# Performance work log

Hardware: AMD Instinct MI355X
Metric: run time of the kernel (lower is better)

## Reference

```python
import jax, jax.numpy as jnp
import numpy as np

SIZE = 640
FPN_STRIDES = (8, 16, 32, 64, 128)
REG_MAX = 16
NUM_CLASSES = 80
TOPK = 45


def _build_anchors():
    pts, boxes, strides = [], [], []
    for s in FPN_STRIDES:
        h, w = SIZE // s, SIZE // s
        y, x = np.meshgrid(np.arange(h), np.arange(w), indexing='ij')
        yf = y.ravel().astype(np.float32)
        xf = x.ravel().astype(np.float32)
        pts.append(np.stack([(yf + 0.5) * s, (xf + 0.5) * s], -1))
        boxes.append(np.stack([yf * s, xf * s, (yf + 1) * s, (xf + 1) * s], -1))
        strides.append(np.full(h * w, s, np.float32))
    return (jnp.asarray(np.concatenate(pts), jnp.float32),
            jnp.asarray(np.concatenate(boxes), jnp.float32),
            jnp.asarray(np.concatenate(strides), jnp.float32))


ANCHOR_PTS, ANCHOR_BOXES, STRIDES = _build_anchors()
NUM_ANCHORS = ANCHOR_PTS.shape[0]  # 8525


def _iou(b1, b2):
    # elementwise IoU over trailing dim 4 in (y1, x1, y2, x2); axes are symmetric
    ty = jnp.maximum(b1[..., 0], b2[..., 0])
    tx = jnp.maximum(b1[..., 1], b2[..., 1])
    by = jnp.minimum(b1[..., 2], b2[..., 2])
    bx = jnp.minimum(b1[..., 3], b2[..., 3])
    inter = jnp.clip(by - ty, 0.0) * jnp.clip(bx - tx, 0.0)
    a1 = (b1[..., 2] - b1[..., 0]) * (b1[..., 3] - b1[..., 1])
    a2 = (b2[..., 2] - b2[..., 0]) * (b2[..., 3] - b2[..., 1])
    return inter / (a1 + a2 - inter)


def _assign_single(gt_cls, gt_bbox, pred_d):
    # gt_cls: (N,), gt_bbox: (N,4), pred_d: (4,A)
    A, N, C = NUM_ANCHORS, gt_bbox.shape[0], NUM_CLASSES
    pts, boxes, strides = ANCHOR_PTS, ANCHOR_BOXES, STRIDES
    centers = (gt_bbox[:, :2] + gt_bbox[:, 2:]) / 2
    dist = jnp.linalg.norm(centers[:, None, :] - pts[None, :, :], axis=-1)  # (N,A)
    _, k_ind = jax.lax.top_k(-dist, TOPK)  # (N,K) nearest anchors
    kb = boxes[k_ind]  # (N,K,4)
    Dg = _iou(gt_bbox[:, None, :], kb)  # (N,K)
    tg = Dg.mean(1) + Dg.std(1, ddof=1)  # torch .std() is unbiased
    ap = pts[k_ind]  # (N,K,2)
    inside = ((gt_bbox[:, None, 0] <= ap[..., 0]) & (ap[..., 0] <= gt_bbox[:, None, 2]) &
              (gt_bbox[:, None, 1] <= ap[..., 1]) & (ap[..., 1] <= gt_bbox[:, None, 3]))
    valid = (Dg >= tg[:, None]) & inside  # (N,K)
    n_idx = jnp.broadcast_to(jnp.arange(N, dtype=jnp.int32)[:, None], (N, TOPK))
    pri = jnp.where(valid, n_idx, -1).ravel()
    a_flat = k_ind.ravel()
    win_d = jnp.full((A,), -1, jnp.int32).at[a_flat].max(pri)
    wb = gt_bbox[jnp.clip(win_d, 0)]  # (A,4)
    gt_d = jnp.stack([(pts[:, 0] - wb[:, 0]) / strides,
                      (pts[:, 1] - wb[:, 1]) / strides,
                      (wb[:, 2] - pts[:, 0]) / strides,
                      (wb[:, 3] - pts[:, 1]) / strides], 0)  # (4,A) = [dtop,dleft,dbottom,dright]
    gt_dfl = jnp.where(win_d[None, :] >= 0, gt_d, jnp.inf)
    cls_pair = gt_cls.astype(jnp.int32)[n_idx]  # (N,K)
    ca = (cls_pair * A + k_ind).ravel()
    win_q = jnp.full((C * A,), -1, jnp.int32).at[ca].max(pri).reshape(C, A)
    gbq = gt_bbox[jnp.clip(win_q, 0)]  # (C,A,4)
    # _overlap_tlbr: decode(gt_d)*stride around anchor point, clamped -> clipped gt box
    box1 = jnp.clip(gbq, 0.0, float(SIZE))  # (C,A,4)
    rd = pred_d * strides[None, :]  # (4,A) raw offsets
    box2 = jnp.stack([jnp.clip(pts[:, 0] - rd[0], 0.0, float(SIZE)),
                      jnp.clip(pts[:, 1] - rd[1], 0.0, float(SIZE)),
                      jnp.clip(pts[:, 0] + rd[2], 0.0, float(SIZE)),
                      jnp.clip(pts[:, 1] + rd[3], 0.0, float(SIZE))], -1)  # (A,4)
    q = _iou(box1, box2[None, :, :])  # (C,A)
    gt_qfl = jnp.where(win_q >= 0, q, 0.0)
    return gt_qfl, gt_dfl


def setup_inputs() -> dict:
    key = jax.random.key(0)
    k1, k2, k3, k4 = jax.random.split(key, 4)
    B, N = 16, 64
    tl = jax.random.uniform(k1, (B, N, 2), jnp.float32, 0.0, SIZE - 64.0)
    wh = jax.random.uniform(k2, (B, N, 2), jnp.float32, 16.0, 256.0)
    br = jnp.minimum(tl + wh, float(SIZE))
    gt_bboxes = jnp.concatenate([tl, br], -1)  # (y1,x1,y2,x2)
    gt_clses = jax.random.randint(k3, (B, N), 0, NUM_CLASSES)
    pred_reg = jax.random.normal(k4, (B, 4, REG_MAX + 1, NUM_ANCHORS), jnp.float32)
    return {"gt_clses_batch": gt_clses, "gt_bboxes_batch": gt_bboxes,
            "pred_reg_batch": pred_reg}


def reference(gt_clses_batch, gt_bboxes_batch, pred_reg_batch):
    p = jax.nn.softmax(pred_reg_batch, axis=2)
    rng = jnp.arange(REG_MAX + 1, dtype=p.dtype).reshape(1, 1, -1, 1)
    pred_d = (p * rng).sum(2)  # (B,4,A) integral distribution -> expected offsets
    qfl, dfl = jax.vmap(_assign_single)(gt_clses_batch, gt_bboxes_batch, pred_d)
    return qfl, dfl, ANCHOR_PTS, STRIDES
```

## Files before the change

### kernel.cpp

```cpp
#include <hip/hip_runtime.h>
#include <math.h>
#include <float.h>

#define A_TOTAL 8525
#define NUM_B   16
#define NUM_N   64
#define NUM_C   80
#define K_TOP   45
#define SIZE_F  640.0f

#define UNASSIGNED_SENTINEL 1.0e30f

#define CUTOFF_KEY 0x43000000u
#define NBINS      2144
#define NBINS_PAD  2304
#define CAND_MAX   768

__device__ __forceinline__ void anchor_decode(int a, float& py, float& px, float& s,
                                              float& qy0, float& qx0, float& qy1, float& qx1) {
    int rel, w; float sf;
    if (a < 6400)      { rel = a;        w = 80; sf = 8.f;   }
    else if (a < 8000) { rel = a - 6400; w = 40; sf = 16.f;  }
    else if (a < 8400) { rel = a - 8000; w = 20; sf = 32.f;  }
    else if (a < 8500) { rel = a - 8400; w = 10; sf = 64.f;  }
    else               { rel = a - 8500; w = 5;  sf = 128.f; }
    int y = rel / w, x = rel - y * w;
    float yf = (float)y, xf = (float)x;
    py  = (yf + 0.5f) * sf;  px  = (xf + 0.5f) * sf;
    qy0 = yf * sf;           qx0 = xf * sf;
    qy1 = (yf + 1.f) * sf;   qx1 = (xf + 1.f) * sf;
    s = sf;
}

__device__ __forceinline__ unsigned int dist_key(int i, float cy, float cx) {
    float py, px, s, q0, q1, q2, q3;
    anchor_decode(i, py, px, s, q0, q1, q2, q3);
    float dy = __fadd_rn(cy, -py);
    float dx = __fadd_rn(cx, -px);
    float v = sqrtf(__fadd_rn(__fmul_rn(dy, dy), __fmul_rn(dx, dx)));
    return __float_as_uint(v);
}

__device__ __forceinline__ float iou_box(float ay0, float ax0, float ay1, float ax1,
                                         float by0, float bx0, float by1, float bx1) {
    float ty = fmaxf(ay0, by0), tx = fmaxf(ax0, bx0);
    float by = fminf(ay1, by1), bx = fminf(ax1, bx1);
    float ih = fmaxf(__fadd_rn(by, -ty), 0.f);
    float iw = fmaxf(__fadd_rn(bx, -tx), 0.f);
    float inter = __fmul_rn(ih, iw);
    float a1 = __fmul_rn(__fadd_rn(ay1, -ay0), __fadd_rn(ax1, -ax0));
    float a2 = __fmul_rn(__fadd_rn(by1, -by0), __fadd_rn(bx1, -bx0));
    return inter / __fadd_rn(__fadd_rn(a1, a2), -inter);
}

__global__ void zero_mask(unsigned long long* __restrict__ mask, int n) {
    int i = blockIdx.x * 256 + threadIdx.x;
    if (i < n) mask[i] = 0ull;
}

__global__ void write_anchors(float* __restrict__ opts, float* __restrict__ ostr) {
    int a = blockIdx.x * 256 + threadIdx.x;
    if (a >= A_TOTAL) return;
    float py, px, s, q0, q1, q2, q3;
    anchor_decode(a, py, px, s, q0, q1, q2, q3);
    opts[2 * a]     = py;
    opts[2 * a + 1] = px;
    ostr[a]         = s;
}

__global__ __launch_bounds__(256) void assign_kernel(const float* __restrict__ gt_bbox,
                                                     unsigned long long* __restrict__ mask) {
    __shared__ unsigned int hist[NBINS_PAD];
    __shared__ unsigned int wtot[4];
    __shared__ unsigned int cand_key[CAND_MAX];
    __shared__ int          cand_idx[CAND_MAX];
    __shared__ int          s_candn;
    __shared__ int          s_B;
    __shared__ int          sel[K_TOP];
    __shared__ float        dg[K_TOP];
    __shared__ float        s_tg;

    int tid = threadIdx.x;
    int lane = tid & 63, wid = tid >> 6;
    int b = blockIdx.x >> 6;
    int n = blockIdx.x & 63;
    const float* gb = gt_bbox + (size_t)(b * NUM_N + n) * 4;
    float g0 = gb[0], g1 = gb[1], g2 = gb[2], g3 = gb[3];
    float cy = __fmul_rn(__fadd_rn(g0, g2), 0.5f);
    float cx = __fmul_rn(__fadd_rn(g1, g3), 0.5f);

    for (int i = tid; i < NBINS_PAD; i += 256) hist[i] = 0u;
    if (tid == 0) s_candn = 0;
    __syncthreads();

    for (int i = tid; i < A_TOTAL; i += 256) {
        unsigned int key = dist_key(i, cy, cx);
        if (key < CUTOFF_KEY) atomicAdd(&hist[key >> 19], 1u);
    }
    __syncthreads();

    unsigned int psum = 0;
    int base = tid * 9;
#pragma unroll
    for (int k = 0; k < 9; ++k) psum += hist[base + k];
    unsigned int x = psum;
    for (int off = 1; off < 64; off <<= 1) {
        unsigned int y = __shfl_up(x, off, 64);
        if (lane >= off) x += y;
    }
    if (lane == 63) wtot[wid] = x;
    __syncthreads();
    unsigned int wbase = 0;
    for (int w = 0; w < 4; ++w) wbase += (w < wid) ? wtot[w] : 0u;
    unsigned int inc = wbase + x;
    unsigned int exc = inc - psum;
    if (exc < (unsigned)K_TOP && inc >= (unsigned)K_TOP) {
        unsigned int cum = exc;
        int bbin = base;
        while (cum + hist[bbin] < (unsigned)K_TOP) { cum += hist[bbin]; ++bbin; }
        s_B = bbin;
    }
    __syncthreads();

    int B = s_B;
    for (int i = tid; i < A_TOTAL; i += 256) {
        unsigned int key = dist_key(i, cy, cx);
        if (key < CUTOFF_KEY && (int)(key >> 19) <= B) {
            int pos = atomicAdd(&s_candn, 1);
            if (pos < CAND_MAX) { cand_key[pos] = key; cand_idx[pos] = i; }
        }
    }
    __syncthreads();

    int M = s_candn < CAND_MAX ? s_candn : CAND_MAX;
    for (int i = tid; i < M; i += 256) {
        unsigned int ki = cand_key[i]; int ii = cand_idx[i];
        int rank = 0;
        for (int j = 0; j < M; ++j) {
            unsigned int kj = cand_key[j]; int ij = cand_idx[j];
            rank += (kj < ki || (kj == ki && ij < ii)) ? 1 : 0;
        }
        if (rank < K_TOP) sel[rank] = ii;
    }
    __syncthreads();

    if (tid < K_TOP) {
        int a = sel[tid];
        float py, px, s, q0, q1, q2, q3;
        anchor_decode(a, py, px, s, q0, q1, q2, q3);
        dg[tid] = iou_box(g0, g1, g2, g3, q0, q1, q2, q3);
    }
    __syncthreads();
    if (tid == 0) {
        float sum = 0.f;
        for (int k = 0; k < K_TOP; ++k) sum = __fadd_rn(sum, dg[k]);
        float mean = sum / (float)K_TOP;
        float ss = 0.f;
        for (int k = 0; k < K_TOP; ++k) {
            float d = __fadd_rn(dg[k], -mean);
            ss = __fadd_rn(ss, __fmul_rn(d, d));
        }
        s_tg = __fadd_rn(mean, sqrtf(ss / (float)(K_TOP - 1)));
    }
    __syncthreads();
    if (tid < K_TOP) {
        int a = sel[tid];
        float py, px, s, q0, q1, q2, q3;
        anchor_decode(a, py, px, s, q0, q1, q2, q3);
        bool inside = (g0 <= py) && (py <= g2) && (g1 <= px) && (px <= g3);
        if (inside && dg[tid] >= s_tg) {
            atomicOr(&mask[(size_t)b * A_TOTAL + a], 1ull << n);
        }
    }
}

__global__ __launch_bounds__(256) void output_kernel(const int* __restrict__ gt_cls,
                                                     const float* __restrict__ gt_bbox,
                                                     const float* __restrict__ pred_reg,
                                                     const unsigned long long* __restrict__ mask,
                                                     float* __restrict__ qfl,
                                                     float* __restrict__ dfl) {
    __shared__ float s_gb[NUM_N * 4];
    __shared__ float s_gc[NUM_N * 4];
    __shared__ int   s_cls[NUM_N];

    int tid = threadIdx.x;
    int b = blockIdx.y;
    if (tid < NUM_N * 4) {
        float v = gt_bbox[(size_t)b * NUM_N * 4 + tid];
        s_gb[tid] = v;
        s_gc[tid] = fminf(fmaxf(v, 0.f), SIZE_F);
    }
    if (tid < NUM_N) s_cls[tid] = gt_cls[b * NUM_N + tid];
    __syncthreads();

    int a = blockIdx.x * 256 + tid;
    if (a >= A_TOTAL) return;

    float py, px, s, q0, q1, q2, q3;
    anchor_decode(a, py, px, s, q0, q1, q2, q3);

    float rd[4];
    const float* pr = pred_reg + (size_t)b * 4 * 17 * A_TOTAL + a;
#pragma unroll
    for (int d = 0; d < 4; ++d) {
        float xv[17];
#pragma unroll
        for (int j = 0; j < 17; ++j) xv[j] = pr[(size_t)(d * 17 + j) * A_TOTAL];
        float m = xv[0];
#pragma unroll
        for (int j = 1; j < 17; ++j) m = fmaxf(m, xv[j]);
        float S = 0.f, dot = 0.f;
#pragma unroll
        for (int j = 0; j < 17; ++j) {
            float t = __expf(xv[j] - m);
            S += t;
            dot += t * (float)j;
        }
        rd[d] = (dot / S) * s;
    }
    float b2y0 = fminf(fmaxf(py - rd[0], 0.f), SIZE_F);
    float b2x0 = fminf(fmaxf(px - rd[1], 0.f), SIZE_F);
    float b2y1 = fminf(fmaxf(py + rd[2], 0.f), SIZE_F);
    float b2x1 = fminf(fmaxf(px + rd[3], 0.f), SIZE_F);

    unsigned long long m64 = mask[(size_t)b * A_TOTAL + a];

    float* dflp = dfl + (size_t)b * 4 * A_TOTAL + a;
    if (m64) {
        int n = 63 - __clzll(m64);
        dflp[0]            = (py - s_gb[n * 4 + 0]) / s;
        dflp[A_TOTAL]      = (px - s_gb[n * 4 + 1]) / s;
        dflp[2 * A_TOTAL]  = (s_gb[n * 4 + 2] - py) / s;
        dflp[3 * A_TOTAL]  = (s_gb[n * 4 + 3] - px) / s;
    } else {
        dflp[0]           = UNASSIGNED_SENTINEL;
        dflp[A_TOTAL]     = UNASSIGNED_SENTINEL;
        dflp[2 * A_TOTAL] = UNASSIGNED_SENTINEL;
        dflp[3 * A_TOTAL] = UNASSIGNED_SENTINEL;
    }

    float* qflp = qfl + (size_t)b * NUM_C * A_TOTAL + a;
#pragma unroll
    for (int c = 0; c < NUM_C; ++c) qflp[(size_t)c * A_TOTAL] = 0.f;

    unsigned long long seen0 = 0ull, seen1 = 0ull;
    unsigned long long mm = m64;
    while (mm) {
        int n = 63 - __clzll(mm);
        mm &= ~(1ull << n);
        int c = s_cls[n];
        bool done;
        if (c < 64) {
            unsigned long long bit = 1ull << c;
            done = (seen0 & bit) != 0ull; seen0 |= bit;
        } else {
            unsigned long long bit = 1ull << (c - 64);
            done = (seen1 & bit) != 0ull; seen1 |= bit;
        }
        if (!done) {
            qflp[(size_t)c * A_TOTAL] = iou_box(s_gc[n * 4 + 0], s_gc[n * 4 + 1],
                                                s_gc[n * 4 + 2], s_gc[n * 4 + 3],
                                                b2y0, b2x0, b2y1, b2x1);
        }
    }
}

extern "C" void kernel_launch(void* const* d_in, const int* in_sizes, int n_in,
                              void* d_out, int out_size, void* d_ws, size_t ws_size,
                              hipStream_t stream) {
    const int*   gt_cls   = (const int*)d_in[0];
    const float* gt_bbox  = (const float*)d_in[1];
    const float* pred_reg = (const float*)d_in[2];

    float* qfl  = (float*)d_out;
    float* dfl  = qfl + (size_t)NUM_B * NUM_C * A_TOTAL;
    float* opts = dfl + (size_t)NUM_B * 4 * A_TOTAL;
    float* ostr = opts + (size_t)A_TOTAL * 2;

    unsigned long long* mask = (unsigned long long*)d_ws;

    int nmask = NUM_B * A_TOTAL;
    hipLaunchKernelGGL(zero_mask, dim3((nmask + 255) / 256), dim3(256), 0, stream, mask, nmask);
    hipLaunchKernelGGL(write_anchors, dim3((A_TOTAL + 255) / 256), dim3(256), 0, stream, opts, ostr);
    hipLaunchKernelGGL(assign_kernel, dim3(NUM_B * NUM_N), dim3(256), 0, stream, gt_bbox, mask);
    hipLaunchKernelGGL(output_kernel, dim3((A_TOTAL + 255) / 256, NUM_B), dim3(256), 0, stream,
                       gt_cls, gt_bbox, pred_reg, mask, qfl, dfl);
}
```

Measured before the change: 135.6 us.

## Fuse prep kernels, bulk-zero qfl upfront, and skip softmax for unassigned anchors

Merges the mask-zero and anchor-write kernels into a single grid-stride prep kernel that also zeroes the whole qfl output with float4 stores. The output kernel now exits early for anchors with an empty assignment mask, writing only the dfl sentinels. That skips the pred_reg softmax loads and the 80 strided zero stores per anchor. The cost is an extra full pass of vectorized qfl zeroing, and because qfl is written by two kernels, the output kernel depends on the prep kernel having run first.

```diff
diff --git a/kernel.cpp b/kernel.cpp
--- a/kernel.cpp
+++ b/kernel.cpp
@@ -15,6 +15,11 @@
 #define NBINS      2144
 #define NBINS_PAD  2304
 #define CAND_MAX   768
+
+#define QFL_FLOATS  ((size_t)NUM_B * NUM_C * A_TOTAL)
+#define QFL_VEC4    (QFL_FLOATS / 4)
+#define MASK_WORDS  (NUM_B * A_TOTAL)
+#define MASK_VEC4   ((MASK_WORDS * 2) / 4)
 
 __device__ __forceinline__ void anchor_decode(int a, float& py, float& px, float& s,
                                               float& qy0, float& qx0, float& qy1, float& qx1) {
@@ -53,19 +58,28 @@
     return inter / __fadd_rn(__fadd_rn(a1, a2), -inter);
 }
 
-__global__ void zero_mask(unsigned long long* __restrict__ mask, int n) {
-    int i = blockIdx.x * 256 + threadIdx.x;
-    if (i < n) mask[i] = 0ull;
-}
-
-__global__ void write_anchors(float* __restrict__ opts, float* __restrict__ ostr) {
-    int a = blockIdx.x * 256 + threadIdx.x;
-    if (a >= A_TOTAL) return;
-    float py, px, s, q0, q1, q2, q3;
-    anchor_decode(a, py, px, s, q0, q1, q2, q3);
-    opts[2 * a]     = py;
-    opts[2 * a + 1] = px;
-    ostr[a]         = s;
+__global__ __launch_bounds__(256) void prep_kernel(float* __restrict__ qfl,
+                                                   unsigned long long* __restrict__ mask,
+                                                   float* __restrict__ opts,
+                                                   float* __restrict__ ostr) {
+    size_t gid = (size_t)blockIdx.x * 256 + threadIdx.x;
+    size_t nthreads = (size_t)gridDim.x * 256;
+
+    float4* q4 = (float4*)qfl;
+    for (size_t i = gid; i < QFL_VEC4; i += nthreads)
+        q4[i] = make_float4(0.f, 0.f, 0.f, 0.f);
+
+    uint4* m4 = (uint4*)mask;
+    for (size_t i = gid; i < MASK_VEC4; i += nthreads)
+        m4[i] = make_uint4(0u, 0u, 0u, 0u);
+
+    for (size_t a = gid; a < A_TOTAL; a += nthreads) {
+        float py, px, s, q0, q1, q2, q3;
+        anchor_decode((int)a, py, px, s, q0, q1, q2, q3);
+        opts[2 * a]     = py;
+        opts[2 * a + 1] = px;
+        ostr[a]         = s;
+    }
 }
 
 __global__ __launch_bounds__(256) void assign_kernel(const float* __restrict__ gt_bbox,
@@ -197,6 +211,17 @@
     int a = blockIdx.x * 256 + tid;
     if (a >= A_TOTAL) return;
 
+    unsigned long long m64 = mask[(size_t)b * A_TOTAL + a];
+    float* dflp = dfl + (size_t)b * 4 * A_TOTAL + a;
+
+    if (m64 == 0ull) {
+        dflp[0]           = UNASSIGNED_SENTINEL;
+        dflp[A_TOTAL]     = UNASSIGNED_SENTINEL;
+        dflp[2 * A_TOTAL] = UNASSIGNED_SENTINEL;
+        dflp[3 * A_TOTAL] = UNASSIGNED_SENTINEL;
+        return;
+    }
+
     float py, px, s, q0, q1, q2, q3;
     anchor_decode(a, py, px, s, q0, q1, q2, q3);
 
@@ -224,26 +249,15 @@
     float b2y1 = fminf(fmaxf(py + rd[2], 0.f), SIZE_F);
     float b2x1 = fminf(fmaxf(px + rd[3], 0.f), SIZE_F);
 
-    unsigned long long m64 = mask[(size_t)b * A_TOTAL + a];
-
-    float* dflp = dfl + (size_t)b * 4 * A_TOTAL + a;
-    if (m64) {
+    {
         int n = 63 - __clzll(m64);
         dflp[0]            = (py - s_gb[n * 4 + 0]) / s;
         dflp[A_TOTAL]      = (px - s_gb[n * 4 + 1]) / s;
         dflp[2 * A_TOTAL]  = (s_gb[n * 4 + 2] - py) / s;
         dflp[3 * A_TOTAL]  = (s_gb[n * 4 + 3] - px) / s;
-    } else {
-        dflp[0]           = UNASSIGNED_SENTINEL;
-        dflp[A_TOTAL]     = UNASSIGNED_SENTINEL;
-        dflp[2 * A_TOTAL] = UNASSIGNED_SENTINEL;
-        dflp[3 * A_TOTAL] = UNASSIGNED_SENTINEL;
     }
 
     float* qflp = qfl + (size_t)b * NUM_C * A_TOTAL + a;
-#pragma unroll
-    for (int c = 0; c < NUM_C; ++c) qflp[(size_t)c * A_TOTAL] = 0.f;
-
     unsigned long long seen0 = 0ull, seen1 = 0ull;
     unsigned long long mm = m64;
     while (mm) {
@@ -274,15 +288,13 @@
     const float* pred_reg = (const float*)d_in[2];
 
     float* qfl  = (float*)d_out;
-    float* dfl  = qfl + (size_t)NUM_B * NUM_C * A_TOTAL;
+    float* dfl  = qfl + QFL_FLOATS;
     float* opts = dfl + (size_t)NUM_B * 4 * A_TOTAL;
     float* ostr = opts + (size_t)A_TOTAL * 2;
 
     unsigned long long* mask = (unsigned long long*)d_ws;
 
-    int nmask = NUM_B * A_TOTAL;
-    hipLaunchKernelGGL(zero_mask, dim3((nmask + 255) / 256), dim3(256), 0, stream, mask, nmask);
-    hipLaunchKernelGGL(write_anchors, dim3((A_TOTAL + 255) / 256), dim3(256), 0, stream, opts, ostr);
+    hipLaunchKernelGGL(prep_kernel, dim3(2048), dim3(256), 0, stream, qfl, mask, opts, ostr);
     hipLaunchKernelGGL(assign_kernel, dim3(NUM_B * NUM_N), dim3(256), 0, stream, gt_bbox, mask);
     hipLaunchKernelGGL(output_kernel, dim3((A_TOTAL + 255) / 256, NUM_B), dim3(256), 0, stream,
                        gt_cls, gt_bbox, pred_reg, mask, qfl, dfl);
```

After: 131.5 us. -3.0%, faster.
